# Kernel optimization log

Hardware: AMD Instinct MI355X
Metric: run time of the kernel (lower is better)

## Reference

```python
import jax, jax.numpy as jnp
import numpy as np

T, B, D, H = 256, 64, 512, 1024


def setup_inputs() -> dict:
    key = jax.random.key(0)
    ks = jax.random.split(key, 9)
    scale = 1.0 / np.sqrt(D + H)  # torch Linear default U(-1/sqrt(fan_in), 1/sqrt(fan_in))
    def lin(k):
        kw, kb = jax.random.split(k)
        W = jax.random.uniform(kw, (H, D + H), jnp.float32, -scale, scale)
        b = jax.random.uniform(kb, (H,), jnp.float32, -scale, scale)
        return W, b
    Wf, bf = lin(ks[0])
    Wi, bi = lin(ks[1])
    Wg, bg = lin(ks[2])
    Wo, bo = lin(ks[3])
    inputs = jax.random.normal(ks[4], (T, B, D), jnp.float32)
    return {"inputs": inputs, "Wf": Wf, "bf": bf, "Wi": Wi, "bi": bi,
            "Wg": Wg, "bg": bg, "Wo": Wo, "bo": bo}


def _lstm(inputs, Wf, bf, Wi, bi, Wg, bg, Wo, bo):
    # Stack the 4 gate linears into one GEMM: W_all [4H, D+H], b_all [4H]
    W_all = jnp.concatenate([Wf, Wi, Wg, Wo], axis=0)
    b_all = jnp.concatenate([bf, bi, bg, bo], axis=0)
    h0 = jnp.zeros((inputs.shape[1], Wf.shape[0]), inputs.dtype)
    c0 = jnp.zeros_like(h0)

    def step(carry, x):
        hx, cx = carry
        combined = jnp.concatenate([x, hx], axis=1)          # [B, D+H]
        gates = combined @ W_all.T + b_all                   # [B, 4H]
        f, i, g, o = jnp.split(gates, 4, axis=1)
        f = jax.nn.sigmoid(f)
        i = jax.nn.sigmoid(i)
        g = jnp.tanh(g)
        o = jax.nn.sigmoid(o)
        cx = f * cx + i * g
        hx = o * jnp.tanh(cx)
        return (hx, cx), hx

    (hT, cT), outputs = jax.lax.scan(step, (h0, c0), inputs)
    return outputs, (hT, cT)


def reference(inputs, Wf, bf, Wi, bi, Wg, bg, Wo, bo):
    return _lstm(inputs, Wf, bf, Wi, bi, Wg, bg, Wo, bo)
```

## Files before the change

kernel.cpp:

```cpp
#include <hip/hip_runtime.h>

#define T_STEPS 256
#define BATCH   64
#define DIN     512
#define HID     1024
#define KTOT    1536
#define NBLK    128
#define NPB     32
#define WPITCH  1544

#define OWNER(bl) ((((bl) & 7) << 4) | ((bl) >> 3))

typedef __attribute__((ext_vector_type(8))) short short8;
typedef __attribute__((ext_vector_type(4))) float f32x4;
typedef __attribute__((ext_vector_type(4))) int   i32x4;

#define WS_WPACK 0
#define WS_XBF   12648448
#define WS_HBF   29425664
#define WS_BPK   29687808
#define WS_SLOTS 29704192
#define WS_HRING 29704704
#define WS_NEED_RING 63390208ULL

#define MFMA(acc, a, b) acc = __builtin_amdgcn_mfma_f32_16x16x32_bf16(a, b, acc, 0, 0, 0)

#define GLD_U(D, P, OFF) \
  asm volatile("global_load_dwordx4 %0, %1, off offset:" #OFF " sc0 sc1" \
               : "=v"(D) : "v"(P))
#define GLD_C(D, P, OFF) \
  asm volatile("global_load_dwordx4 %0, %1, off offset:" #OFF \
               : "=v"(D) : "v"(P))
#define TIE(N, x0, x1, x2, x3, x4, x5, x6, x7) \
  asm volatile("s_waitcnt vmcnt(" #N ")" \
               : "+v"(x0), "+v"(x1), "+v"(x2), "+v"(x3), \
                 "+v"(x4), "+v"(x5), "+v"(x6), "+v"(x7))

#define HGEMM_BODY(GLD) do { \
      i32x4 p0, p1, p2, p3, p4, p5, p6, p7; \
      i32x4 q0, q1, q2, q3, q4, q5, q6, q7; \
      GLD(p0, hb, 0);    GLD(p1, hb, 64);   GLD(p2, hb, 128);  GLD(p3, hb, 192); \
      GLD(p4, hb, 256);  GLD(p5, hb, 320);  GLD(p6, hb, 384);  GLD(p7, hb, 448); \
      GLD(q0, hb, 512);  GLD(q1, hb, 576);  GLD(q2, hb, 640);  GLD(q3, hb, 704); \
      GLD(q4, hb, 768);  GLD(q5, hb, 832);  GLD(q6, hb, 896);  GLD(q7, hb, 960); \
      TIE(8, p0, p1, p2, p3, p4, p5, p6, p7); \
      consume8(p0, p1, p2, p3, p4, p5, p6, p7, 0); \
      GLD(p0, hb, 1024); GLD(p1, hb, 1088); GLD(p2, hb, 1152); GLD(p3, hb, 1216); \
      GLD(p4, hb, 1280); GLD(p5, hb, 1344); GLD(p6, hb, 1408); GLD(p7, hb, 1472); \
      TIE(8, q0, q1, q2, q3, q4, q5, q6, q7); \
      consume8(q0, q1, q2, q3, q4, q5, q6, q7, 8); \
      GLD(q0, hb, 1536); GLD(q1, hb, 1600); GLD(q2, hb, 1664); GLD(q3, hb, 1728); \
      GLD(q4, hb, 1792); GLD(q5, hb, 1856); GLD(q6, hb, 1920); GLD(q7, hb, 1984); \
      TIE(8, p0, p1, p2, p3, p4, p5, p6, p7); \
      consume8(p0, p1, p2, p3, p4, p5, p6, p7, 16); \
      TIE(0, q0, q1, q2, q3, q4, q5, q6, q7); \
      consume8(q0, q1, q2, q3, q4, q5, q6, q7, 24); \
    } while (0)

__device__ inline unsigned short f2bf(float x) {
  unsigned u = __builtin_bit_cast(unsigned, x);
  u += 0x7FFF + ((u >> 16) & 1);
  return (unsigned short)(u >> 16);
}

__global__ void prep_x(const float* __restrict__ x, ushort* __restrict__ Xbf,
                       ushort* __restrict__ hbf, ushort* __restrict__ hring,
                       unsigned* __restrict__ slots,
                       const float* __restrict__ bfv, const float* __restrict__ biv,
                       const float* __restrict__ bgv, const float* __restrict__ bov,
                       float* __restrict__ bpack) {
  unsigned i = blockIdx.x * 256 + threadIdx.x;
  float4 v = ((const float4*)x)[i];
  ushort4 o = make_ushort4(f2bf(v.x), f2bf(v.y), f2bf(v.z), f2bf(v.w));
  ((ushort4*)Xbf)[i] = o;
  if (i < (2 * BATCH * HID) / 4) ((ushort4*)hbf)[i] = make_ushort4(0, 0, 0, 0);
  if (i < (BATCH * HID) / 4) ((ushort4*)hring)[i] = make_ushort4(0, 0, 0, 0);
  if (i < NBLK * NPB) {
    int bl = i >> 5, n = i & 31, gate = n >> 3, jj = n & 7;
    int j = OWNER(bl) * 8 + jj;
    const float* b = (gate == 0) ? bfv : (gate == 1) ? biv : (gate == 2) ? bgv : bov;
    bpack[i] = b[j];
  }
  if (i < NBLK) slots[i] = 0;
}

__global__ void prep_w(const float* __restrict__ Wf, const float* __restrict__ Wi,
                       const float* __restrict__ Wg, const float* __restrict__ Wo,
                       ushort* __restrict__ Wpack) {
  int row = blockIdx.x;
  int bl = row >> 5, n = row & 31, gate = n >> 3, jj = n & 7;
  int j = OWNER(bl) * 8 + jj;
  const float* src = ((gate == 0) ? Wf : (gate == 1) ? Wi : (gate == 2) ? Wg : Wo)
                     + (size_t)j * KTOT;
  ushort* dst = Wpack + (size_t)row * WPITCH;
  for (int idx = threadIdx.x; idx < KTOT / 4; idx += 256) {
    float4 v = ((const float4*)src)[idx];
    ((ushort4*)dst)[idx] = make_ushort4(f2bf(v.x), f2bf(v.y), f2bf(v.z), f2bf(v.w));
  }
}

template <bool RING>
__launch_bounds__(256)
__global__ void lstm_persist(const ushort* __restrict__ Wpack,
                             const ushort* __restrict__ Xbf,
                             ushort* __restrict__ hbf,
                             ushort* __restrict__ hring,
                             const float* __restrict__ bpack,
                             unsigned* __restrict__ slots,
                             float* __restrict__ out) {
  __shared__ __align__(16) ushort Wlds[NPB * WPITCH];
  __shared__ float gates[NPB][BATCH + 4];
  __shared__ float blds[NPB];
  __shared__ float clds[8][BATCH + 1];

  const int tid  = threadIdx.x;
  const int bl   = blockIdx.x;
  const int lane = tid & 63;
  const int wave = tid >> 6;
  const int jbase = OWNER(bl) * 8;

  {
    const uint4* src = (const uint4*)(Wpack + (size_t)bl * NPB * WPITCH);
    uint4* dst = (uint4*)Wlds;
    for (int i = tid; i < NPB * WPITCH / 8; i += 256) dst[i] = src[i];
  }
  if (tid < NPB) blds[tid] = bpack[bl * NPB + tid];
  for (int i = tid; i < 8 * (BATCH + 1); i += 256) (&clds[0][0])[i] = 0.f;
  __syncthreads();

  const int m0    = wave * 16 + (lane & 15);
  const int kgrp8 = (lane >> 4) * 8;
  const ushort* wx0 = Wlds + (lane & 15) * WPITCH + kgrp8;
  const ushort* wx1 = wx0 + 16 * WPITCH;
  const ushort* wh0 = wx0 + DIN;
  const ushort* wh1 = wx1 + DIN;

  const f32x4 vzero = {0.f, 0.f, 0.f, 0.f};
  f32x4 acc00 = vzero, acc01 = vzero, acc10 = vzero, acc11 = vzero;

  auto xpart = [&](int t) {
    acc00 = vzero; acc01 = vzero; acc10 = vzero; acc11 = vzero;
    const ushort* xp = Xbf + ((size_t)t * BATCH + m0) * DIN + kgrp8;
#pragma unroll
    for (int ki = 0; ki < 16; ++ki) {
      short8 a  = *(const short8*)(xp + ki * 32);
      short8 b0 = *(const short8*)(wx0 + ki * 32);
      short8 b1 = *(const short8*)(wx1 + ki * 32);
      if (ki & 1) { MFMA(acc01, a, b0); MFMA(acc11, a, b1); }
      else        { MFMA(acc00, a, b0); MFMA(acc10, a, b1); }
    }
  };
  auto consume8 = [&](i32x4 v0, i32x4 v1, i32x4 v2, i32x4 v3,
                      i32x4 v4, i32x4 v5, i32x4 v6, i32x4 v7, int kiBase) {
    const ushort* b0p = wh0 + kiBase * 32;
    const ushort* b1p = wh1 + kiBase * 32;
    MFMA(acc00, __builtin_bit_cast(short8, v0), *(const short8*)(b0p + 0 * 32));
    MFMA(acc10, __builtin_bit_cast(short8, v0), *(const short8*)(b1p + 0 * 32));
    MFMA(acc01, __builtin_bit_cast(short8, v1), *(const short8*)(b0p + 1 * 32));
    MFMA(acc11, __builtin_bit_cast(short8, v1), *(const short8*)(b1p + 1 * 32));
    MFMA(acc00, __builtin_bit_cast(short8, v2), *(const short8*)(b0p + 2 * 32));
    MFMA(acc10, __builtin_bit_cast(short8, v2), *(const short8*)(b1p + 2 * 32));
    MFMA(acc01, __builtin_bit_cast(short8, v3), *(const short8*)(b0p + 3 * 32));
    MFMA(acc11, __builtin_bit_cast(short8, v3), *(const short8*)(b1p + 3 * 32));
    MFMA(acc00, __builtin_bit_cast(short8, v4), *(const short8*)(b0p + 4 * 32));
    MFMA(acc10, __builtin_bit_cast(short8, v4), *(const short8*)(b1p + 4 * 32));
    MFMA(acc01, __builtin_bit_cast(short8, v5), *(const short8*)(b0p + 5 * 32));
    MFMA(acc11, __builtin_bit_cast(short8, v5), *(const short8*)(b1p + 5 * 32));
    MFMA(acc00, __builtin_bit_cast(short8, v6), *(const short8*)(b0p + 6 * 32));
    MFMA(acc10, __builtin_bit_cast(short8, v6), *(const short8*)(b1p + 6 * 32));
    MFMA(acc01, __builtin_bit_cast(short8, v7), *(const short8*)(b0p + 7 * 32));
    MFMA(acc11, __builtin_bit_cast(short8, v7), *(const short8*)(b1p + 7 * 32));
  };

  xpart(0);
  for (int t = 0; t < T_STEPS; ++t) {
    if (tid < 64) {
      const unsigned tu = (unsigned)t;
      for (;;) {
        unsigned v0 = __hip_atomic_load(&slots[lane],      __ATOMIC_RELAXED, __HIP_MEMORY_SCOPE_AGENT);
        unsigned v1 = __hip_atomic_load(&slots[lane + 64], __ATOMIC_RELAXED, __HIP_MEMORY_SCOPE_AGENT);
        if (__all((v0 >= tu) && (v1 >= tu))) break;
        __builtin_amdgcn_s_sleep(1);
      }
    }
    __syncthreads();

    {
      const ushort* hb;
      if (RING) hb = hring + (size_t)t * (BATCH * HID) + (size_t)m0 * HID + kgrp8;
      else      hb = hbf + (size_t)(t & 1) * (BATCH * HID) + (size_t)m0 * HID + kgrp8;
      if (RING) HGEMM_BODY(GLD_C);
      else      HGEMM_BODY(GLD_U);
    }

    {
      f32x4 g0 = acc00 + acc01, g1 = acc10 + acc11;
      int n0 = lane & 15;
      int mq = wave * 16 + (lane >> 4) * 4;
      *(f32x4*)&gates[n0][mq]      = g0;
      *(f32x4*)&gates[16 + n0][mq] = g1;
    }
    __syncthreads();

    if (tid < BATCH) {
      const int m = tid;
      float h8[8], c8[8];
#pragma unroll
      for (int jj = 0; jj < 8; ++jj) {
        float fp = gates[jj][m]      + blds[jj];
        float ip = gates[8 + jj][m]  + blds[8 + jj];
        float gp = gates[16 + jj][m] + blds[16 + jj];
        float op = gates[24 + jj][m] + blds[24 + jj];
        float fs = 1.f / (1.f + __expf(-fp));
        float is = 1.f / (1.f + __expf(-ip));
        float os = 1.f / (1.f + __expf(-op));
        float gt = 1.f - 2.f / (__expf(2.f * gp) + 1.f);
        float c  = fs * clds[jj][m] + is * gt;
        clds[jj][m] = c;
        float th = 1.f - 2.f / (__expf(2.f * c) + 1.f);
        h8[jj] = os * th;
        c8[jj] = c;
      }
      unsigned long long hl = (unsigned long long)f2bf(h8[0])
                            | ((unsigned long long)f2bf(h8[1]) << 16)
                            | ((unsigned long long)f2bf(h8[2]) << 32)
                            | ((unsigned long long)f2bf(h8[3]) << 48);
      unsigned long long hh = (unsigned long long)f2bf(h8[4])
                            | ((unsigned long long)f2bf(h8[5]) << 16)
                            | ((unsigned long long)f2bf(h8[6]) << 32)
                            | ((unsigned long long)f2bf(h8[7]) << 48);
      ushort* hdst;
      if (RING) hdst = hring + (size_t)(t + 1) * (BATCH * HID);
      else      hdst = hbf + (size_t)((t + 1) & 1) * (BATCH * HID);
      unsigned long long* hp64 =
          (unsigned long long*)(hdst + (size_t)m * HID + jbase);
      __hip_atomic_store(hp64,     hl, __ATOMIC_RELAXED, __HIP_MEMORY_SCOPE_AGENT);
      __hip_atomic_store(hp64 + 1, hh, __ATOMIC_RELAXED, __HIP_MEMORY_SCOPE_AGENT);
      asm volatile("s_waitcnt vmcnt(0)" ::: "memory");
      if (tid == 0)
        __hip_atomic_store(&slots[bl], (unsigned)(t + 1),
                           __ATOMIC_RELAXED, __HIP_MEMORY_SCOPE_AGENT);
      float* op0 = out + (size_t)t * (BATCH * HID) + (size_t)m * HID + jbase;
      *(float4*)op0       = make_float4(h8[0], h8[1], h8[2], h8[3]);
      *(float4*)(op0 + 4) = make_float4(h8[4], h8[5], h8[6], h8[7]);
      if (t == T_STEPS - 1) {
        float* hp = out + (size_t)T_STEPS * BATCH * HID + (size_t)m * HID + jbase;
        float* cp = hp + BATCH * HID;
        *(float4*)hp       = make_float4(h8[0], h8[1], h8[2], h8[3]);
        *(float4*)(hp + 4) = make_float4(h8[4], h8[5], h8[6], h8[7]);
        *(float4*)cp       = make_float4(c8[0], c8[1], c8[2], c8[3]);
        *(float4*)(cp + 4) = make_float4(c8[4], c8[5], c8[6], c8[7]);
      }
    }

    if (t < T_STEPS - 1) xpart(t + 1);
  }
}

extern "C" void kernel_launch(void* const* d_in, const int* in_sizes, int n_in,
                              void* d_out, int out_size, void* d_ws, size_t ws_size,
                              hipStream_t stream) {
  const float* x   = (const float*)d_in[0];
  const float* Wf  = (const float*)d_in[1];
  const float* bfv = (const float*)d_in[2];
  const float* Wi  = (const float*)d_in[3];
  const float* biv = (const float*)d_in[4];
  const float* Wg  = (const float*)d_in[5];
  const float* bgv = (const float*)d_in[6];
  const float* Wo  = (const float*)d_in[7];
  const float* bov = (const float*)d_in[8];

  char* ws = (char*)d_ws;
  ushort*   Wpack = (ushort*)(ws + WS_WPACK);
  ushort*   Xbf   = (ushort*)(ws + WS_XBF);
  ushort*   hbf   = (ushort*)(ws + WS_HBF);
  float*    bpack = (float*)(ws + WS_BPK);
  unsigned* slots = (unsigned*)(ws + WS_SLOTS);
  ushort*   hring = (ushort*)(ws + WS_HRING);
  float*    out   = (float*)d_out;

  const bool ring = (ws_size >= WS_NEED_RING);
  if (!ring) hring = hbf;

  prep_x<<<dim3((T_STEPS * BATCH * DIN) / 4 / 256), dim3(256), 0, stream>>>(
      x, Xbf, hbf, hring, slots, bfv, biv, bgv, bov, bpack);
  prep_w<<<dim3(NBLK * NPB), dim3(256), 0, stream>>>(Wf, Wi, Wg, Wo, Wpack);

  const ushort* Wpc = Wpack;
  const ushort* Xbc = Xbf;
  const float*  bpc = bpack;
  void* args[] = {(void*)&Wpc, (void*)&Xbc, (void*)&hbf, (void*)&hring,
                  (void*)&bpc, (void*)&slots, (void*)&out};
  if (ring)
    hipLaunchCooperativeKernel((const void*)&lstm_persist<true>, dim3(NBLK),
                               dim3(256), args, 0, stream);
  else
    hipLaunchCooperativeKernel((const void*)&lstm_persist<false>, dim3(NBLK),
                               dim3(256), args, 0, stream);
}
```

Before: 2.164 ms.

## Spread LSTM cell update across all waves and overlap flag polling with x-part GEMM

The elementwise cell update moves from the first 64 threads doing 8 columns each to all four waves doing 2 columns each, with a block barrier before the completion flag is published. The inter-block wait moves to the end of each step: wave 0 issues cache-bypassing flag loads, then the next step's input-projection GEMM runs, and only afterwards does it spin on the flags. This is meant to hide the grid-wide synchronisation latency behind independent work and shorten the serial critical path per timestep. It adds an extra __syncthreads per step and uses narrower 32-bit h stores.

Measured after the change: 2.460 ms. +13.7%, slower.

```diff
diff --git a/kernel.cpp b/kernel.cpp
--- a/kernel.cpp
+++ b/kernel.cpp
@@ -174,17 +174,6 @@
 
   xpart(0);
   for (int t = 0; t < T_STEPS; ++t) {
-    if (tid < 64) {
-      const unsigned tu = (unsigned)t;
-      for (;;) {
-        unsigned v0 = __hip_atomic_load(&slots[lane],      __ATOMIC_RELAXED, __HIP_MEMORY_SCOPE_AGENT);
-        unsigned v1 = __hip_atomic_load(&slots[lane + 64], __ATOMIC_RELAXED, __HIP_MEMORY_SCOPE_AGENT);
-        if (__all((v0 >= tu) && (v1 >= tu))) break;
-        __builtin_amdgcn_s_sleep(1);
-      }
-    }
-    __syncthreads();
-
     {
       const ushort* hb;
       if (RING) hb = hring + (size_t)t * (BATCH * HID) + (size_t)m0 * HID + kgrp8;
@@ -202,11 +191,13 @@
     }
     __syncthreads();
 
-    if (tid < BATCH) {
-      const int m = tid;
-      float h8[8], c8[8];
+    {
+      const int m  = tid & 63;
+      const int c0 = 2 * wave;
+      float h2[2], c2[2];
 #pragma unroll
-      for (int jj = 0; jj < 8; ++jj) {
+      for (int u = 0; u < 2; ++u) {
+        int jj = c0 + u;
         float fp = gates[jj][m]      + blds[jj];
         float ip = gates[8 + jj][m]  + blds[8 + jj];
         float gp = gates[16 + jj][m] + blds[16 + jj];
@@ -218,42 +209,51 @@
         float c  = fs * clds[jj][m] + is * gt;
         clds[jj][m] = c;
         float th = 1.f - 2.f / (__expf(2.f * c) + 1.f);
-        h8[jj] = os * th;
-        c8[jj] = c;
+        h2[u] = os * th;
+        c2[u] = c;
       }
-      unsigned long long hl = (unsigned long long)f2bf(h8[0])
-                            | ((unsigned long long)f2bf(h8[1]) << 16)
-                            | ((unsigned long long)f2bf(h8[2]) << 32)
-                            | ((unsigned long long)f2bf(h8[3]) << 48);
-      unsigned long long hh = (unsigned long long)f2bf(h8[4])
-                            | ((unsigned long long)f2bf(h8[5]) << 16)
-                            | ((unsigned long long)f2bf(h8[6]) << 32)
-                            | ((unsigned long long)f2bf(h8[7]) << 48);
+      unsigned hword = (unsigned)f2bf(h2[0]) | ((unsigned)f2bf(h2[1]) << 16);
       ushort* hdst;
       if (RING) hdst = hring + (size_t)(t + 1) * (BATCH * HID);
       else      hdst = hbf + (size_t)((t + 1) & 1) * (BATCH * HID);
-      unsigned long long* hp64 =
-          (unsigned long long*)(hdst + (size_t)m * HID + jbase);
-      __hip_atomic_store(hp64,     hl, __ATOMIC_RELAXED, __HIP_MEMORY_SCOPE_AGENT);
-      __hip_atomic_store(hp64 + 1, hh, __ATOMIC_RELAXED, __HIP_MEMORY_SCOPE_AGENT);
+      unsigned* hp32 = (unsigned*)(hdst + (size_t)m * HID + jbase + c0);
+      __hip_atomic_store(hp32, hword, __ATOMIC_RELAXED, __HIP_MEMORY_SCOPE_AGENT);
       asm volatile("s_waitcnt vmcnt(0)" ::: "memory");
+      __syncthreads();
       if (tid == 0)
         __hip_atomic_store(&slots[bl], (unsigned)(t + 1),
                            __ATOMIC_RELAXED, __HIP_MEMORY_SCOPE_AGENT);
-      float* op0 = out + (size_t)t * (BATCH * HID) + (size_t)m * HID + jbase;
-      *(float4*)op0       = make_float4(h8[0], h8[1], h8[2], h8[3]);
-      *(float4*)(op0 + 4) = make_float4(h8[4], h8[5], h8[6], h8[7]);
+      float* op0 = out + (size_t)t * (BATCH * HID) + (size_t)m * HID + jbase + c0;
+      *(float2*)op0 = make_float2(h2[0], h2[1]);
       if (t == T_STEPS - 1) {
-        float* hp = out + (size_t)T_STEPS * BATCH * HID + (size_t)m * HID + jbase;
+        float* hp = out + (size_t)T_STEPS * BATCH * HID + (size_t)m * HID + jbase + c0;
         float* cp = hp + BATCH * HID;
-        *(float4*)hp       = make_float4(h8[0], h8[1], h8[2], h8[3]);
-        *(float4*)(hp + 4) = make_float4(h8[4], h8[5], h8[6], h8[7]);
-        *(float4*)cp       = make_float4(c8[0], c8[1], c8[2], c8[3]);
-        *(float4*)(cp + 4) = make_float4(c8[4], c8[5], c8[6], c8[7]);
+        *(float2*)hp = make_float2(h2[0], h2[1]);
+        *(float2*)cp = make_float2(c2[0], c2[1]);
       }
     }
 
-    if (t < T_STEPS - 1) xpart(t + 1);
+    if (t < T_STEPS - 1) {
+      unsigned s0 = 0, s1 = 0;
+      const unsigned* sp = slots + lane;
+      if (wave == 0) {
+        asm volatile("global_load_dword %0, %1, off sc0 sc1"
+                     : "=v"(s0) : "v"(sp));
+        asm volatile("global_load_dword %0, %1, off offset:256 sc0 sc1"
+                     : "=v"(s1) : "v"(sp));
+      }
+      xpart(t + 1);
+      if (wave == 0) {
+        asm volatile("s_waitcnt vmcnt(0)" : "+v"(s0), "+v"(s1));
+        const unsigned tu = (unsigned)(t + 1);
+        while (!__all((s0 >= tu) && (s1 >= tu))) {
+          __builtin_amdgcn_s_sleep(1);
+          s0 = __hip_atomic_load(&slots[lane],      __ATOMIC_RELAXED, __HIP_MEMORY_SCOPE_AGENT);
+          s1 = __hip_atomic_load(&slots[lane + 64], __ATOMIC_RELAXED, __HIP_MEMORY_SCOPE_AGENT);
+        }
+      }
+      __syncthreads();
+    }
   }
 }
 
```
